# Performance work log

Hardware: AMD Instinct MI355X
Metric: run time of the kernel (lower is better)

Reference implementation:

```python
import jax, jax.numpy as jnp
import numpy as np

N_NODES = 50000
N_EDGES = 800000
D_IN = 64
D_OUT = 64


def setup_inputs() -> dict:
    key = jax.random.key(0)
    k1, k2, k3, k4, k5 = jax.random.split(key, 5)
    features = jax.random.normal(k1, (N_NODES, D_IN), dtype=jnp.float32)
    edge_src = jax.random.randint(k2, (N_EDGES,), 0, N_NODES, dtype=jnp.int32)
    edge_dst = jax.random.randint(k3, (N_EDGES,), 0, N_NODES, dtype=jnp.int32)
    edge_weight = jax.random.uniform(k4, (N_EDGES,), dtype=jnp.float32)
    # Linear(2*D_IN, D_OUT): weight [D_OUT, 2*D_IN], bias [D_OUT]
    W = jax.random.normal(k5, (D_OUT, 2 * D_IN), dtype=jnp.float32) * (1.0 / np.sqrt(2 * D_IN))
    b = jnp.zeros((D_OUT,), dtype=jnp.float32)
    return {"features": features, "edge_src": edge_src, "edge_dst": edge_dst,
            "edge_weight": edge_weight, "W": W, "b": b}


def reference(features, edge_src, edge_dst, edge_weight, W, b):
    n = features.shape[0]
    # spmm(adj, features): out[i] = sum_j adj[i,j] * features[j]
    gathered = features[edge_src] * edge_weight[:, None]          # [E, D_IN]
    neighbor = jax.ops.segment_sum(gathered, edge_dst, num_segments=n)  # [N, D_IN]
    combined = jnp.concatenate([features, neighbor], axis=1)     # [N, 2*D_IN]
    out = combined @ W.T + b                                      # [N, D_OUT]
    # F.normalize(p=2, dim=1): x / max(||x||, 1e-12)
    norm = jnp.maximum(jnp.linalg.norm(out, axis=1, keepdims=True), 1e-12)
    return out / norm
```

## Files before the change

kernel.cpp:

```cpp
#include <hip/hip_runtime.h>

#define D 64
#define TILE 1024
#define RB 8
#define EPB 2048
#define EPT 8

__device__ __forceinline__ float rlane(float v, int l) {
    return __int_as_float(__builtin_amdgcn_readlane(__float_as_int(v), l));
}

__global__ __launch_bounds__(256) void hist_kernel(
    const int* __restrict__ edge_dst, int* __restrict__ deg,
    int n_edges, int n_nodes)
{
    __shared__ int s_cnt;
    __shared__ int s_d[EPB];
    int r = blockIdx.x & (RB - 1);
    int chunk = blockIdx.x >> 3;
    int lo = (int)((long long)r * n_nodes / RB);
    int hi = (int)((long long)(r + 1) * n_nodes / RB);
    if (threadIdx.x == 0) s_cnt = 0;
    __syncthreads();

    int base = chunk * EPB + threadIdx.x * EPT;
    int d[EPT];
    if (base + EPT - 1 < n_edges) {
        int4 v0 = *(const int4*)(edge_dst + base);
        int4 v1 = *(const int4*)(edge_dst + base + 4);
        d[0]=v0.x; d[1]=v0.y; d[2]=v0.z; d[3]=v0.w;
        d[4]=v1.x; d[5]=v1.y; d[6]=v1.z; d[7]=v1.w;
    } else {
        #pragma unroll
        for (int k = 0; k < EPT; ++k)
            d[k] = (base + k < n_edges) ? edge_dst[base + k] : -1;
    }

    int lane = threadIdx.x & 63;
    unsigned long long lt = (lane == 63) ? ~0ull >> 1
                                         : ((1ull << (lane + 1)) - 1) >> 1;
    #pragma unroll
    for (int k = 0; k < EPT; ++k) {
        bool m = (d[k] >= lo && d[k] < hi);
        unsigned long long bal = __ballot(m);
        int cw = __popcll(bal);
        if (cw) {
            int bs = 0;
            if (lane == 0) bs = atomicAdd(&s_cnt, cw);
            bs = __builtin_amdgcn_readfirstlane(bs);
            if (m) s_d[bs + __popcll(bal & lt)] = d[k];
        }
    }
    __syncthreads();
    int c = s_cnt;
    for (int i = threadIdx.x; i < c; i += 256) atomicAdd(&deg[s_d[i]], 1);
}

__global__ __launch_bounds__(256) void tile_sum_kernel(
    const int* __restrict__ deg, int* __restrict__ partial, int n)
{
    int t = threadIdx.x;
    int base = blockIdx.x * TILE + t * 4;
    int s = 0;
    if (base + 3 < n) {
        int4 v = *(const int4*)(deg + base);
        s = v.x + v.y + v.z + v.w;
    } else {
        for (int k = 0; k < 4; ++k) if (base + k < n) s += deg[base + k];
    }
    #pragma unroll
    for (int off = 1; off < 64; off <<= 1) s += __shfl_xor(s, off, 64);
    __shared__ int wsum[4];
    int lane = t & 63, wv = t >> 6;
    if (lane == 0) wsum[wv] = s;
    __syncthreads();
    if (t == 0) partial[blockIdx.x] = wsum[0] + wsum[1] + wsum[2] + wsum[3];
}

__global__ __launch_bounds__(64) void scan_partial_kernel(
    const int* __restrict__ partial, int* __restrict__ ppref, int nb,
    int* __restrict__ offsets, int n, int n_edges)
{
    int lane = threadIdx.x;
    int carry = 0;
    for (int base = 0; base < nb; base += 64) {
        int idx = base + lane;
        int v = (idx < nb) ? partial[idx] : 0;
        int inc = v;
        #pragma unroll
        for (int off = 1; off < 64; off <<= 1) {
            int u = __shfl_up(inc, off, 64);
            if (lane >= off) inc += u;
        }
        if (idx < nb) ppref[idx] = carry + inc - v;
        carry += __shfl(inc, 63, 64);
    }
    if (lane == 0) offsets[n] = n_edges;
}

__global__ __launch_bounds__(256) void scan_tile_kernel(
    const int* __restrict__ deg, const int* __restrict__ ppref,
    int* __restrict__ offsets, int* __restrict__ cursor, int n)
{
    int t = threadIdx.x;
    int base = blockIdx.x * TILE + t * 4;
    int e0 = 0, e1 = 0, e2 = 0, e3 = 0;
    if (base + 3 < n) {
        int4 v = *(const int4*)(deg + base);
        e0 = v.x; e1 = v.y; e2 = v.z; e3 = v.w;
    } else {
        if (base + 0 < n) e0 = deg[base + 0];
        if (base + 1 < n) e1 = deg[base + 1];
        if (base + 2 < n) e2 = deg[base + 2];
        if (base + 3 < n) e3 = deg[base + 3];
    }
    int s = e0 + e1 + e2 + e3;
    int inc = s;
    int lane = t & 63, wv = t >> 6;
    #pragma unroll
    for (int off = 1; off < 64; off <<= 1) {
        int u = __shfl_up(inc, off, 64);
        if (lane >= off) inc += u;
    }
    __shared__ int wsum[4];
    if (lane == 63) wsum[wv] = inc;
    __syncthreads();
    int wpre = 0;
    for (int wq = 0; wq < wv; ++wq) wpre += wsum[wq];
    int excl = ppref[blockIdx.x] + wpre + inc - s;
    int o0 = excl, o1 = o0 + e0, o2 = o1 + e1, o3 = o2 + e2;
    if (base + 0 < n) { offsets[base + 0] = o0; cursor[base + 0] = o0; }
    if (base + 1 < n) { offsets[base + 1] = o1; cursor[base + 1] = o1; }
    if (base + 2 < n) { offsets[base + 2] = o2; cursor[base + 2] = o2; }
    if (base + 3 < n) { offsets[base + 3] = o3; cursor[base + 3] = o3; }
}

__global__ __launch_bounds__(256) void fill_kernel(
    const int* __restrict__ edge_src, const int* __restrict__ edge_dst,
    const float* __restrict__ edge_weight,
    int* __restrict__ cursor, int2* __restrict__ csr_sw,
    int n_edges, int n_nodes)
{
    __shared__ int s_cnt;
    __shared__ int s_d[EPB];
    __shared__ int s_e[EPB];
    int r = blockIdx.x & (RB - 1);
    int chunk = blockIdx.x >> 3;
    int lo = (int)((long long)r * n_nodes / RB);
    int hi = (int)((long long)(r + 1) * n_nodes / RB);
    if (threadIdx.x == 0) s_cnt = 0;
    __syncthreads();

    int base = chunk * EPB + threadIdx.x * EPT;
    int d[EPT];
    if (base + EPT - 1 < n_edges) {
        int4 v0 = *(const int4*)(edge_dst + base);
        int4 v1 = *(const int4*)(edge_dst + base + 4);
        d[0]=v0.x; d[1]=v0.y; d[2]=v0.z; d[3]=v0.w;
        d[4]=v1.x; d[5]=v1.y; d[6]=v1.z; d[7]=v1.w;
    } else {
        #pragma unroll
        for (int k = 0; k < EPT; ++k)
            d[k] = (base + k < n_edges) ? edge_dst[base + k] : -1;
    }

    int lane = threadIdx.x & 63;
    unsigned long long lt = (lane == 63) ? ~0ull >> 1
                                         : ((1ull << (lane + 1)) - 1) >> 1;
    #pragma unroll
    for (int k = 0; k < EPT; ++k) {
        bool m = (d[k] >= lo && d[k] < hi);
        unsigned long long bal = __ballot(m);
        int cw = __popcll(bal);
        if (cw) {
            int bs = 0;
            if (lane == 0) bs = atomicAdd(&s_cnt, cw);
            bs = __builtin_amdgcn_readfirstlane(bs);
            if (m) {
                int p = bs + __popcll(bal & lt);
                s_d[p] = d[k];
                s_e[p] = base + k;
            }
        }
    }
    __syncthreads();
    int c = s_cnt;
    for (int i = threadIdx.x; i < c; i += 256) {
        int dk = s_d[i];
        int e  = s_e[i];
        int pos = atomicAdd(&cursor[dk], 1);
        csr_sw[pos] = make_int2(edge_src[e], __float_as_int(edge_weight[e]));
    }
}

__global__ __launch_bounds__(256) void gather_kernel(
    const float* __restrict__ features, const int2* __restrict__ csr_sw,
    const int* __restrict__ offsets, float* __restrict__ neighbor, int n_nodes)
{
    int lane = threadIdx.x & 63;
    int gw = (blockIdx.x * 256 + threadIdx.x) >> 6;
    int nw = (gridDim.x * 256) >> 6;
    for (int i = gw; i < n_nodes; i += nw) {
        int beg = __builtin_amdgcn_readfirstlane(offsets[i]);
        int end = __builtin_amdgcn_readfirstlane(offsets[i + 1]);
        float acc = 0.f;
        int j = beg;
        for (; j + 7 < end; j += 8) {
            int2 p[8];
            float a[8];
            #pragma unroll
            for (int q = 0; q < 8; ++q) p[q] = csr_sw[j + q];
            #pragma unroll
            for (int q = 0; q < 8; ++q)
                a[q] = features[(size_t)p[q].x * D + lane];
            #pragma unroll
            for (int q = 0; q < 8; ++q)
                acc = fmaf(__int_as_float(p[q].y), a[q], acc);
        }
        for (; j < end; ++j) {
            int2 p = csr_sw[j];
            acc = fmaf(__int_as_float(p.y), features[(size_t)p.x * D + lane], acc);
        }
        neighbor[(size_t)i * D + lane] = acc;
    }
}

__global__ __launch_bounds__(256) void gemm_norm_kernel(
    const float* __restrict__ features, const float* __restrict__ neighbor,
    const float* __restrict__ W, const float* __restrict__ bias,
    float* __restrict__ out, int n_nodes)
{
    __shared__ float4 Wt4[32][64];
    int tid = threadIdx.x;
    #pragma unroll
    for (int idx = tid; idx < 32 * 64; idx += 256) {
        int k4 = idx >> 6, o = idx & 63;
        Wt4[k4][o] = *(const float4*)(W + (size_t)o * 128 + k4 * 4);
    }
    __syncthreads();

    int lane = tid & 63;
    int wv = tid >> 6;
    float bl = bias[lane];

    int g = blockIdx.x * 4 + wv;
    int i0 = g * 8;
    if (i0 >= n_nodes) return;
    int cnt = min(8, n_nodes - i0);

    float cf[8], cn[8], acc[8];
    #pragma unroll
    for (int t = 0; t < 8; ++t) {
        int i = i0 + ((t < cnt) ? t : 0);
        cf[t] = features[(size_t)i * D + lane];
        cn[t] = neighbor[(size_t)i * D + lane];
        acc[t] = bl;
    }

    #pragma unroll 4
    for (int k4 = 0; k4 < 16; ++k4) {
        float4 w4 = Wt4[k4][lane];
        int kb = 4 * k4;
        #pragma unroll
        for (int t = 0; t < 8; ++t) {
            acc[t] = fmaf(rlane(cf[t], kb + 0), w4.x, acc[t]);
            acc[t] = fmaf(rlane(cf[t], kb + 1), w4.y, acc[t]);
            acc[t] = fmaf(rlane(cf[t], kb + 2), w4.z, acc[t]);
            acc[t] = fmaf(rlane(cf[t], kb + 3), w4.w, acc[t]);
        }
    }
    #pragma unroll 4
    for (int k4 = 16; k4 < 32; ++k4) {
        float4 w4 = Wt4[k4][lane];
        int kb = 4 * k4 - 64;
        #pragma unroll
        for (int t = 0; t < 8; ++t) {
            acc[t] = fmaf(rlane(cn[t], kb + 0), w4.x, acc[t]);
            acc[t] = fmaf(rlane(cn[t], kb + 1), w4.y, acc[t]);
            acc[t] = fmaf(rlane(cn[t], kb + 2), w4.z, acc[t]);
            acc[t] = fmaf(rlane(cn[t], kb + 3), w4.w, acc[t]);
        }
    }

    #pragma unroll
    for (int t = 0; t < 8; ++t) {
        if (t < cnt) {
            float s = acc[t] * acc[t];
            #pragma unroll
            for (int m = 1; m < 64; m <<= 1) s += __shfl_xor(s, m, 64);
            out[(size_t)(i0 + t) * D + lane] = acc[t] / fmaxf(sqrtf(s), 1e-12f);
        }
    }
}

extern "C" void kernel_launch(void* const* d_in, const int* in_sizes, int n_in,
                              void* d_out, int out_size, void* d_ws, size_t ws_size,
                              hipStream_t stream) {
    const float* features    = (const float*)d_in[0];
    const int*   edge_src    = (const int*)d_in[1];
    const int*   edge_dst    = (const int*)d_in[2];
    const float* edge_weight = (const float*)d_in[3];
    const float* W           = (const float*)d_in[4];
    const float* b           = (const float*)d_in[5];
    float*       out         = (float*)d_out;

    int n = in_sizes[0] / D;
    int E = in_sizes[1];
    int nb = (n + TILE - 1) / TILE;
    int nchunks = (E + EPB - 1) / EPB;

    char* ws = (char*)d_ws;
    auto al = [](size_t x) { return (x + 255) & ~(size_t)255; };
    size_t o = 0;
    int* deg      = (int*)(ws + o); o += al((size_t)n * 4);
    int* cursor   = (int*)(ws + o); o += al((size_t)n * 4);
    int* offsets  = (int*)(ws + o); o += al((size_t)(n + 1) * 4);
    int* partial  = (int*)(ws + o); o += al((size_t)nb * 4);
    int* ppref    = (int*)(ws + o); o += al((size_t)nb * 4);
    int2* csr_sw  = (int2*)(ws + o); o += al((size_t)E * 8);
    float* neighbor = (float*)(ws + o);

    hipMemsetAsync(deg, 0, (size_t)n * 4, stream);

    hist_kernel<<<nchunks * RB, 256, 0, stream>>>(edge_dst, deg, E, n);
    tile_sum_kernel<<<nb, 256, 0, stream>>>(deg, partial, n);
    scan_partial_kernel<<<1, 64, 0, stream>>>(partial, ppref, nb, offsets, n, E);
    scan_tile_kernel<<<nb, 256, 0, stream>>>(deg, ppref, offsets, cursor, n);
    fill_kernel<<<nchunks * RB, 256, 0, stream>>>(edge_src, edge_dst, edge_weight,
                                                  cursor, csr_sw, E, n);
    gather_kernel<<<2048, 256, 0, stream>>>(features, csr_sw, offsets,
                                            neighbor, n);
    int groups = (n + 7) / 8;
    gemm_norm_kernel<<<(groups + 3) / 4, 256, 0, stream>>>(features, neighbor,
                                                           W, b, out, n);
}
```

Baseline: 230.0 us.

## Stage GEMM rows in LDS and use persistent grid-stride blocks

The GEMM+normalize kernel stops broadcasting row values with readlane and instead stores each wave's 8 combined rows in shared memory, reading them as float4 broadcasts. The launch changes from one block per 32 rows to a fixed grid of 512 persistent blocks that loop over row groups, so the W transpose into LDS is paid fewer times. The cost is 16 KB of extra LDS per block, which may lower occupancy. There is also no barrier between reusing the per-wave buffer across iterations, which relies on a wave's lanes running in lockstep.

```diff
diff --git a/kernel.cpp b/kernel.cpp
--- a/kernel.cpp
+++ b/kernel.cpp
@@ -5,10 +5,6 @@
 #define RB 8
 #define EPB 2048
 #define EPT 8
-
-__device__ __forceinline__ float rlane(float v, int l) {
-    return __int_as_float(__builtin_amdgcn_readlane(__float_as_int(v), l));
-}
 
 __global__ __launch_bounds__(256) void hist_kernel(
     const int* __restrict__ edge_dst, int* __restrict__ deg,
@@ -231,8 +227,8 @@
     float* __restrict__ out, int n_nodes)
 {
     __shared__ float4 Wt4[32][64];
+    __shared__ float comb[4][8][128];
     int tid = threadIdx.x;
-    #pragma unroll
     for (int idx = tid; idx < 32 * 64; idx += 256) {
         int k4 = idx >> 6, o = idx & 63;
         Wt4[k4][o] = *(const float4*)(W + (size_t)o * 128 + k4 * 4);
@@ -243,52 +239,44 @@
     int wv = tid >> 6;
     float bl = bias[lane];
 
-    int g = blockIdx.x * 4 + wv;
-    int i0 = g * 8;
-    if (i0 >= n_nodes) return;
-    int cnt = min(8, n_nodes - i0);
-
-    float cf[8], cn[8], acc[8];
-    #pragma unroll
-    for (int t = 0; t < 8; ++t) {
-        int i = i0 + ((t < cnt) ? t : 0);
-        cf[t] = features[(size_t)i * D + lane];
-        cn[t] = neighbor[(size_t)i * D + lane];
-        acc[t] = bl;
-    }
-
-    #pragma unroll 4
-    for (int k4 = 0; k4 < 16; ++k4) {
-        float4 w4 = Wt4[k4][lane];
-        int kb = 4 * k4;
+    int ngroups = (n_nodes + 7) >> 3;
+    for (int g = blockIdx.x * 4 + wv; g < ngroups; g += gridDim.x * 4) {
+        int i0 = g * 8;
+        int cnt = min(8, n_nodes - i0);
+
         #pragma unroll
         for (int t = 0; t < 8; ++t) {
-            acc[t] = fmaf(rlane(cf[t], kb + 0), w4.x, acc[t]);
-            acc[t] = fmaf(rlane(cf[t], kb + 1), w4.y, acc[t]);
-            acc[t] = fmaf(rlane(cf[t], kb + 2), w4.z, acc[t]);
-            acc[t] = fmaf(rlane(cf[t], kb + 3), w4.w, acc[t]);
-        }
-    }
-    #pragma unroll 4
-    for (int k4 = 16; k4 < 32; ++k4) {
-        float4 w4 = Wt4[k4][lane];
-        int kb = 4 * k4 - 64;
+            int i = i0 + ((t < cnt) ? t : 0);
+            comb[wv][t][lane]      = features[(size_t)i * D + lane];
+            comb[wv][t][64 + lane] = neighbor[(size_t)i * D + lane];
+        }
+
+        float acc[8];
+        #pragma unroll
+        for (int t = 0; t < 8; ++t) acc[t] = bl;
+
+        #pragma unroll 4
+        for (int k4 = 0; k4 < 32; ++k4) {
+            float4 w4 = Wt4[k4][lane];
+            #pragma unroll
+            for (int t = 0; t < 8; ++t) {
+                float4 c4 = *(const float4*)&comb[wv][t][4 * k4];
+                acc[t] = fmaf(c4.x, w4.x, acc[t]);
+                acc[t] = fmaf(c4.y, w4.y, acc[t]);
+                acc[t] = fmaf(c4.z, w4.z, acc[t]);
+                acc[t] = fmaf(c4.w, w4.w, acc[t]);
+            }
+        }
+
         #pragma unroll
         for (int t = 0; t < 8; ++t) {
-            acc[t] = fmaf(rlane(cn[t], kb + 0), w4.x, acc[t]);
-            acc[t] = fmaf(rlane(cn[t], kb + 1), w4.y, acc[t]);
-            acc[t] = fmaf(rlane(cn[t], kb + 2), w4.z, acc[t]);
-            acc[t] = fmaf(rlane(cn[t], kb + 3), w4.w, acc[t]);
-        }
-    }
-
-    #pragma unroll
-    for (int t = 0; t < 8; ++t) {
-        if (t < cnt) {
-            float s = acc[t] * acc[t];
-            #pragma unroll
-            for (int m = 1; m < 64; m <<= 1) s += __shfl_xor(s, m, 64);
-            out[(size_t)(i0 + t) * D + lane] = acc[t] / fmaxf(sqrtf(s), 1e-12f);
+            if (t < cnt) {
+                float s = acc[t] * acc[t];
+                #pragma unroll
+                for (int m = 1; m < 64; m <<= 1) s += __shfl_xor(s, m, 64);
+                out[(size_t)(i0 + t) * D + lane] =
+                    acc[t] / fmaxf(sqrtf(s), 1e-12f);
+            }
         }
     }
 }
@@ -330,7 +318,5 @@
                                                   cursor, csr_sw, E, n);
     gather_kernel<<<2048, 256, 0, stream>>>(features, csr_sw, offsets,
                                             neighbor, n);
-    int groups = (n + 7) / 8;
-    gemm_norm_kernel<<<(groups + 3) / 4, 256, 0, stream>>>(features, neighbor,
-                                                           W, b, out, n);
-}
+    gemm_norm_kernel<<<512, 256, 0, stream>>>(features, neighbor, W, b, out, n);
+}
```

After: 228.4 us. No clear change (-0.7%).
